# Performance work log

Hardware: AMD Instinct MI355X
Metric: run time of the kernel (lower is better)

## Reference

```python
import jax, jax.numpy as jnp
import numpy as np

N_Q, N_T, D, C = 4096, 8192, 512, 16
SIGMA = 2.0


def setup_inputs() -> dict:
    key = jax.random.key(0)
    k1, k2, k3 = jax.random.split(key, 3)
    X = jax.random.normal(k1, (N_Q, D), dtype=jnp.float32)
    X_train = jax.random.normal(k2, (N_T, D), dtype=jnp.float32)
    y = jax.random.randint(k3, (N_T,), 0, C, dtype=jnp.int32)
    sigma = jnp.float32(SIGMA)
    return {"X": X, "X_train": X_train, "y": y, "sigma": sigma}


def reference(X, X_train, y, sigma):
    xx = jnp.sum(X * X, axis=1, keepdims=True)              # [N_q, 1]
    tt = jnp.sum(X_train * X_train, axis=1)                 # [N_t]
    cross = jnp.einsum('qd,td->qt', X, X_train)             # [N_q, N_t]
    dist2 = jnp.maximum(xx + tt[None, :] - 2.0 * cross, 0.0)
    pattern = jnp.exp(-dist2 / (2.0 * sigma ** 2))          # Gaussian RBF kernel [N_q, N_t]
    # per-class segment sum over training patterns (replaces per-class Python loop)
    summation = jax.ops.segment_sum(pattern.T, y, num_segments=C).T  # [N_q, C]
    summation = summation / jnp.sum(summation, axis=1, keepdims=True)
    return jnp.argmax(summation, axis=1)
```

## Files before the change

### kernel.cpp

```cpp
#include <hip/hip_runtime.h>


#define NQ 4096
#define NT 8192
#define DD 512
#define NC 16
#define LN_FLT_MIN -87.336544750402f
#define SCREEN_T 750.0f

typedef __attribute__((ext_vector_type(4))) int   v4i;
typedef __attribute__((ext_vector_type(8))) int   v8i;
typedef __attribute__((ext_vector_type(16))) float f32x16;

static __device__ __forceinline__ unsigned f2fp4(float x) {
  const float a = __builtin_fabsf(x);
  unsigned i = (unsigned)(a >= 0.25f) + (a >= 0.75f) + (a >= 1.25f)
             + (a >= 1.75f) + (a >= 2.5f) + (a >= 3.5f) + (a >= 5.0f);
  return i | (x < 0.0f ? 8u : 0u);
}

__global__ __launch_bounds__(256) void prep_k(const float* __restrict__ X,
                                              const float* __restrict__ XT,
                                              unsigned char* __restrict__ fXp,
                                              unsigned char* __restrict__ fTp,
                                              float* __restrict__ xx,
                                              float* __restrict__ tt,
                                              float* __restrict__ classacc) {
  const int lane = threadIdx.x & 63;
  const int row  = blockIdx.x * 4 + (threadIdx.x >> 6);
  const float* src; unsigned char* dst; float* nrm; int r;
  if (row < NT) { r = row; src = XT + (size_t)r * DD; dst = fTp; nrm = tt + r; }
  else { r = row - NT; src = X + (size_t)r * DD; dst = fXp; nrm = xx + r; }
  const float4* s4 = (const float4*)src;
  const float4 a = s4[lane * 2], b = s4[lane * 2 + 1];
  const unsigned word =  f2fp4(a.x)        | (f2fp4(a.y) << 4)
                      | (f2fp4(a.z) << 8)  | (f2fp4(a.w) << 12)
                      | (f2fp4(b.x) << 16) | (f2fp4(b.y) << 20)
                      | (f2fp4(b.z) << 24) | (f2fp4(b.w) << 28);
  const int l = (r & 31) + 32 * ((lane >> 2) & 1);
  const size_t dest = ((size_t)(r >> 5) * 8 + (lane >> 3)) * 1024
                    + l * 16 + (lane & 3) * 4;
  *(unsigned*)(dst + dest) = word;
  float acc = a.x*a.x + a.y*a.y + a.z*a.z + a.w*a.w
            + b.x*b.x + b.y*b.y + b.z*b.z + b.w*b.w;
  #pragma unroll
  for (int off = 32; off; off >>= 1) acc += __shfl_down(acc, off, 64);
  if (lane == 0) *nrm = acc;
  if (blockIdx.x < 64) {
    float4 z = {0.f, 0.f, 0.f, 0.f};
    ((float4*)classacc)[blockIdx.x * 256 + threadIdx.x] = z;
  }
}

#define MFMA4(A, B, C) __builtin_amdgcn_mfma_scale_f32_32x32x64_f8f6f4( \
    (A), (B), (C), 4, 4, 0, 127, 0, 127)
#define BAR() __builtin_amdgcn_s_barrier()
#define WAITV(N) asm volatile("s_waitcnt vmcnt(" #N ")" ::: "memory")

static __device__ __forceinline__ void gll(const unsigned char* src, char* dst) {
  __builtin_amdgcn_global_load_lds(
      (const __attribute__((address_space(1))) unsigned int*)src,
      (__attribute__((address_space(3))) unsigned int*)dst, 16, 0, 0);
}

static __device__ __forceinline__ v8i ld16(const char* p) {
  const v4i lo = *(const v4i*)p;
  return __builtin_shufflevector(lo, lo, 0, 1, 2, 3, -1, -1, -1, -1);
}

__global__ __launch_bounds__(512) void pnn_mfma(const unsigned char* __restrict__ fXp,
                                                const unsigned char* __restrict__ fTp,
                                                const float* __restrict__ Xf,
                                                const float* __restrict__ Tf,
                                                const int* __restrict__ y,
                                                const float* __restrict__ sigp,
                                                const float* __restrict__ xx,
                                                const float* __restrict__ tt,
                                                float* __restrict__ classacc) {
  extern __shared__ char lds[];
  const int tid  = threadIdx.x;
  const int w    = tid >> 6, lane = tid & 63;
  const int la   = lane & 31, lb = lane >> 5;
  const int wr   = w >> 2, wc = w & 3;

  const int bid = blockIdx.x;
  const int xcd = bid & 7, cc = bid >> 3;
  const int qt  = (xcd & 3) * 8 + (cc >> 4);
  const int tn  = (xcd >> 2) * 16 + (cc & 15);
  const int qbase = qt * 128, tbase = tn * 256;
  const int qrt0 = qbase >> 5, trt0 = tbase >> 5;

  const unsigned char* sb0 = fXp + ((size_t)(qrt0 + (w >> 1)) * 8 + (w & 1)) * 1024 + lane * 16;
  const unsigned char* sb1 = fTp + ((size_t)(trt0 + (w >> 1)) * 8 + (w & 1)) * 1024 + lane * 16;
  const unsigned char* sb2 = fTp + ((size_t)(trt0 + 4 + (w >> 1)) * 8 + (w & 1)) * 1024 + lane * 16;
  const int d0 = w * 1024 + lane * 16;
  const int d1 = (w + 8) * 1024 + lane * 16;
  const int d2 = (w + 16) * 1024 + lane * 16;

#define STAGE(s, bofs) { \
    gll(sb0 + (size_t)(s) * 2048, lds + (bofs) + d0); \
    gll(sb1 + (size_t)(s) * 2048, lds + (bofs) + d1); \
    gll(sb2 + (size_t)(s) * 2048, lds + (bofs) + d2); }

  f32x16 acc00 = (f32x16)(0.f), acc01 = (f32x16)(0.f);
  f32x16 acc10 = (f32x16)(0.f), acc11 = (f32x16)(0.f);

  STAGE(0, 0)

  #pragma unroll
  for (int s = 0; s < 4; ++s) {
    const int cur = (s % 3) * 24576;
    const int nxt = ((s + 1) % 3) * 24576;
    if (s < 3) { STAGE(s + 1, nxt) }
    if (s < 3) { WAITV(3); } else { WAITV(0); }
    BAR();
    const char* Bp = lds + cur;
    const v8i a00 = ld16(Bp + ((wr * 2 + 0) * 2 + 0) * 1024 + lane * 16);
    const v8i a10 = ld16(Bp + ((wr * 2 + 1) * 2 + 0) * 1024 + lane * 16);
    const v8i b00 = ld16(Bp + (8 + (wc * 2 + 0) * 2 + 0) * 1024 + lane * 16);
    const v8i b10 = ld16(Bp + (8 + (wc * 2 + 1) * 2 + 0) * 1024 + lane * 16);
    const v8i a01 = ld16(Bp + ((wr * 2 + 0) * 2 + 1) * 1024 + lane * 16);
    const v8i a11 = ld16(Bp + ((wr * 2 + 1) * 2 + 1) * 1024 + lane * 16);
    const v8i b01 = ld16(Bp + (8 + (wc * 2 + 0) * 2 + 1) * 1024 + lane * 16);
    const v8i b11 = ld16(Bp + (8 + (wc * 2 + 1) * 2 + 1) * 1024 + lane * 16);
    __builtin_amdgcn_s_setprio(1);
    acc00 = MFMA4(a00, b00, acc00);
    acc01 = MFMA4(a00, b10, acc01);
    acc10 = MFMA4(a10, b00, acc10);
    acc11 = MFMA4(a10, b10, acc11);
    acc00 = MFMA4(a01, b01, acc00);
    acc01 = MFMA4(a01, b11, acc01);
    acc10 = MFMA4(a11, b01, acc10);
    acc11 = MFMA4(a11, b11, acc11);
    __builtin_amdgcn_s_setprio(0);
  }
#undef STAGE

  const int wq = qbase + wr * 64;
  const int wt = tbase + wc * 64;
  const float sg = sigp[0];
  const float inv2s2 = 1.0f / (2.0f * sg * sg);
  float tnorm[2]; int tcls[2];
  #pragma unroll
  for (int nt = 0; nt < 2; ++nt) {
    const int t = wt + nt * 32 + la;
    tnorm[nt] = tt[t]; tcls[nt] = y[t];
  }

#define EPIL(ACC, mt, nt) { \
    _Pragma("unroll") \
    for (int reg = 0; reg < 16; ++reg) { \
      const int q = wq + (mt) * 32 + (reg & 3) + 8 * (reg >> 2) + 4 * lb; \
      const float xq = xx[q]; \
      const float d2 = xq + tnorm[(nt)] - 2.0f * (ACC)[reg]; \
      if (__builtin_expect(d2 < SCREEN_T, 0)) { \
        const int t = wt + (nt) * 32 + la; \
        const float4* xp = (const float4*)(Xf + (size_t)q * DD); \
        const float4* tp = (const float4*)(Tf + (size_t)t * DD); \
        float s0 = 0.f, s1 = 0.f, s2 = 0.f, s3 = 0.f; \
        for (int d = 0; d < DD / 4; ++d) { \
          const float4 xv = xp[d], tv = tp[d]; \
          s0 = fmaf(xv.x, tv.x, s0); s1 = fmaf(xv.y, tv.y, s1); \
          s2 = fmaf(xv.z, tv.z, s2); s3 = fmaf(xv.w, tv.w, s3); \
        } \
        const float dot = (s0 + s1) + (s2 + s3); \
        const float dd2 = fmaxf(xq + tnorm[(nt)] - 2.0f * dot, 0.f); \
        const float arg = -dd2 * inv2s2; \
        if (arg >= LN_FLT_MIN)             \
          atomicAdd(&classacc[q * NC + tcls[(nt)]], expf(arg)); \
      } \
    } }

  EPIL(acc00, 0, 0)
  EPIL(acc01, 0, 1)
  EPIL(acc10, 1, 0)
  EPIL(acc11, 1, 1)
#undef EPIL
}

__global__ __launch_bounds__(256) void argmax_k(const float* __restrict__ classacc,
                                                float* __restrict__ out) {
  const int q = blockIdx.x * 256 + threadIdx.x;
  float sc[NC];
  #pragma unroll
  for (int c4 = 0; c4 < 4; ++c4) {
    const float4 v = ((const float4*)(classacc + (size_t)q * NC))[c4];
    sc[c4*4+0] = v.x; sc[c4*4+1] = v.y; sc[c4*4+2] = v.z; sc[c4*4+3] = v.w;
  }
  float rowsum = 0.f;
  #pragma unroll
  for (int c = 0; c < NC; ++c) rowsum += sc[c];
  int best = 0; float bv = sc[0];
  #pragma unroll
  for (int c = 1; c < NC; ++c)
    if (sc[c] > bv) { bv = sc[c]; best = c; }
  out[q] = (rowsum > 0.f) ? (float)best : 0.0f;
}

extern "C" void kernel_launch(void* const* d_in, const int* in_sizes, int n_in,
                              void* d_out, int out_size, void* d_ws, size_t ws_size,
                              hipStream_t stream) {
  const float* X  = (const float*)d_in[0];
  const float* XT = (const float*)d_in[1];
  const int*   y  = (const int*)d_in[2];
  const float* sg = (const float*)d_in[3];
  float* out = (float*)d_out;

  char* wsp = (char*)d_ws;
  unsigned char* fXp = (unsigned char*)wsp;
  unsigned char* fTp = fXp + (size_t)NQ * DD / 2;
  float* tt       = (float*)(wsp + 4u * 1024u * 1024u);
  float* xx       = tt + NT;
  float* classacc = xx + NQ;

  (void)hipFuncSetAttribute((const void*)pnn_mfma,
                            hipFuncAttributeMaxDynamicSharedMemorySize, 73728);

  prep_k<<<(NQ + NT) / 4, 256, 0, stream>>>(X, XT, fXp, fTp, xx, tt, classacc);
  pnn_mfma<<<1024, 512, 73728, stream>>>(fXp, fTp, X, XT, y, sg, xx, tt, classacc);
  argmax_k<<<NQ / 256, 256, 0, stream>>>(classacc, out);
}
```

Before: 50.98 us.

## Keep query FP4 tile in registers and loop over training strips per block

Each block now holds its 128-query FP4 A tile in registers for the whole K=512 and iterates over four 256-wide training tiles of a 1024-wide strip. Those B tiles are double-buffered in 128KB of LDS, cutting the grid from 1024 to 256 blocks. The aim is to reuse A across training tiles and overlap the next B load with MFMA and epilogue work, avoiding the per-block restaging of A. The cost is one block per CU, so 256 blocks only partly fill the GPU. It also adds more register pressure and serialises the epilogue with compute inside each block.

```diff
diff --git a/kernel.cpp b/kernel.cpp
--- a/kernel.cpp
+++ b/kernel.cpp
@@ -55,7 +55,7 @@
 #define MFMA4(A, B, C) __builtin_amdgcn_mfma_scale_f32_32x32x64_f8f6f4( \
     (A), (B), (C), 4, 4, 0, 127, 0, 127)
 #define BAR() __builtin_amdgcn_s_barrier()
-#define WAITV(N) asm volatile("s_waitcnt vmcnt(" #N ")" ::: "memory")
+#define WAITV0() asm volatile("s_waitcnt vmcnt(0)" ::: "memory")
 
 static __device__ __forceinline__ void gll(const unsigned char* src, char* dst) {
   __builtin_amdgcn_global_load_lds(
@@ -63,89 +63,82 @@
       (__attribute__((address_space(3))) unsigned int*)dst, 16, 0, 0);
 }
 
-static __device__ __forceinline__ v8i ld16(const char* p) {
-  const v4i lo = *(const v4i*)p;
+static __device__ __forceinline__ v8i pk8(v4i lo) {
   return __builtin_shufflevector(lo, lo, 0, 1, 2, 3, -1, -1, -1, -1);
 }
 
-__global__ __launch_bounds__(512) void pnn_mfma(const unsigned char* __restrict__ fXp,
-                                                const unsigned char* __restrict__ fTp,
-                                                const float* __restrict__ Xf,
-                                                const float* __restrict__ Tf,
-                                                const int* __restrict__ y,
-                                                const float* __restrict__ sigp,
-                                                const float* __restrict__ xx,
-                                                const float* __restrict__ tt,
-                                                float* __restrict__ classacc) {
+__global__ __launch_bounds__(512, 1) void pnn_mfma(const unsigned char* __restrict__ fXp,
+                                                   const unsigned char* __restrict__ fTp,
+                                                   const float* __restrict__ Xf,
+                                                   const float* __restrict__ Tf,
+                                                   const int* __restrict__ y,
+                                                   const float* __restrict__ sigp,
+                                                   const float* __restrict__ xx,
+                                                   const float* __restrict__ tt,
+                                                   float* __restrict__ classacc) {
   extern __shared__ char lds[];
   const int tid  = threadIdx.x;
   const int w    = tid >> 6, lane = tid & 63;
   const int la   = lane & 31, lb = lane >> 5;
   const int wr   = w >> 2, wc = w & 3;
 
-  const int bid = blockIdx.x;
-  const int xcd = bid & 7, cc = bid >> 3;
-  const int qt  = (xcd & 3) * 8 + (cc >> 4);
-  const int tn  = (xcd >> 2) * 16 + (cc & 15);
-  const int qbase = qt * 128, tbase = tn * 256;
-  const int qrt0 = qbase >> 5, trt0 = tbase >> 5;
-
-  const unsigned char* sb0 = fXp + ((size_t)(qrt0 + (w >> 1)) * 8 + (w & 1)) * 1024 + lane * 16;
-  const unsigned char* sb1 = fTp + ((size_t)(trt0 + (w >> 1)) * 8 + (w & 1)) * 1024 + lane * 16;
-  const unsigned char* sb2 = fTp + ((size_t)(trt0 + 4 + (w >> 1)) * 8 + (w & 1)) * 1024 + lane * 16;
-  const int d0 = w * 1024 + lane * 16;
-  const int d1 = (w + 8) * 1024 + lane * 16;
-  const int d2 = (w + 16) * 1024 + lane * 16;
-
-#define STAGE(s, bofs) { \
-    gll(sb0 + (size_t)(s) * 2048, lds + (bofs) + d0); \
-    gll(sb1 + (size_t)(s) * 2048, lds + (bofs) + d1); \
-    gll(sb2 + (size_t)(s) * 2048, lds + (bofs) + d2); }
-
-  f32x16 acc00 = (f32x16)(0.f), acc01 = (f32x16)(0.f);
-  f32x16 acc10 = (f32x16)(0.f), acc11 = (f32x16)(0.f);
-
-  STAGE(0, 0)
-
-  #pragma unroll
-  for (int s = 0; s < 4; ++s) {
-    const int cur = (s % 3) * 24576;
-    const int nxt = ((s + 1) % 3) * 24576;
-    if (s < 3) { STAGE(s + 1, nxt) }
-    if (s < 3) { WAITV(3); } else { WAITV(0); }
-    BAR();
-    const char* Bp = lds + cur;
-    const v8i a00 = ld16(Bp + ((wr * 2 + 0) * 2 + 0) * 1024 + lane * 16);
-    const v8i a10 = ld16(Bp + ((wr * 2 + 1) * 2 + 0) * 1024 + lane * 16);
-    const v8i b00 = ld16(Bp + (8 + (wc * 2 + 0) * 2 + 0) * 1024 + lane * 16);
-    const v8i b10 = ld16(Bp + (8 + (wc * 2 + 1) * 2 + 0) * 1024 + lane * 16);
-    const v8i a01 = ld16(Bp + ((wr * 2 + 0) * 2 + 1) * 1024 + lane * 16);
-    const v8i a11 = ld16(Bp + ((wr * 2 + 1) * 2 + 1) * 1024 + lane * 16);
-    const v8i b01 = ld16(Bp + (8 + (wc * 2 + 0) * 2 + 1) * 1024 + lane * 16);
-    const v8i b11 = ld16(Bp + (8 + (wc * 2 + 1) * 2 + 1) * 1024 + lane * 16);
-    __builtin_amdgcn_s_setprio(1);
-    acc00 = MFMA4(a00, b00, acc00);
-    acc01 = MFMA4(a00, b10, acc01);
-    acc10 = MFMA4(a10, b00, acc10);
-    acc11 = MFMA4(a10, b10, acc11);
-    acc00 = MFMA4(a01, b01, acc00);
-    acc01 = MFMA4(a01, b11, acc01);
-    acc10 = MFMA4(a11, b01, acc10);
-    acc11 = MFMA4(a11, b11, acc11);
-    __builtin_amdgcn_s_setprio(0);
-  }
-#undef STAGE
-
-  const int wq = qbase + wr * 64;
-  const int wt = tbase + wc * 64;
+  const int bid   = blockIdx.x;
+  const int strip = bid & 7;
+  const int qt    = bid >> 3;
+  const int qbase = qt * 128;
+  const int rt0   = (qbase >> 5) + wr * 2;
+
   const float sg = sigp[0];
   const float inv2s2 = 1.0f / (2.0f * sg * sg);
-  float tnorm[2]; int tcls[2];
-  #pragma unroll
-  for (int nt = 0; nt < 2; ++nt) {
-    const int t = wt + nt * 32 + la;
-    tnorm[nt] = tt[t]; tcls[nt] = y[t];
-  }
+  const int wq = qbase + wr * 64;
+
+  v4i av[2][8];
+  #pragma unroll
+  for (int mt = 0; mt < 2; ++mt)
+    #pragma unroll
+    for (int kt = 0; kt < 8; ++kt)
+      av[mt][kt] = *(const v4i*)(fXp + ((size_t)(rt0 + mt) * 8 + kt) * 1024 + lane * 16);
+
+#define STAGEB(buf, trt0) { \
+    _Pragma("unroll") \
+    for (int j = 0; j < 8; ++j) \
+      gll(fTp + ((size_t)((trt0) + j) * 8 + w) * 1024 + lane * 16, \
+          (buf) + (j * 8 + w) * 1024 + lane * 16); }
+
+  char* cur = lds;
+  char* nxt = lds + 65536;
+
+  STAGEB(cur, strip * 32)
+  WAITV0();
+  BAR();
+
+  #pragma clang loop unroll(disable)
+  for (int t = 0; t < 4; ++t) {
+    if (t < 3) STAGEB(nxt, strip * 32 + (t + 1) * 8)
+
+    f32x16 acc00 = (f32x16)(0.f), acc01 = (f32x16)(0.f);
+    f32x16 acc10 = (f32x16)(0.f), acc11 = (f32x16)(0.f);
+
+    #pragma unroll
+    for (int kt = 0; kt < 8; ++kt) {
+      const v4i b0 = *(const v4i*)(cur + ((wc * 2 + 0) * 8 + kt) * 1024 + lane * 16);
+      const v4i b1 = *(const v4i*)(cur + ((wc * 2 + 1) * 8 + kt) * 1024 + lane * 16);
+      const v8i a0 = pk8(av[0][kt]), a1 = pk8(av[1][kt]);
+      const v8i bb0 = pk8(b0), bb1 = pk8(b1);
+      acc00 = MFMA4(a0, bb0, acc00);
+      acc01 = MFMA4(a0, bb1, acc01);
+      acc10 = MFMA4(a1, bb0, acc10);
+      acc11 = MFMA4(a1, bb1, acc11);
+    }
+
+    const int tbase = strip * 1024 + t * 256;
+    const int wt = tbase + wc * 64;
+    float tnorm[2]; int tcls[2];
+    #pragma unroll
+    for (int nt = 0; nt < 2; ++nt) {
+      const int tg = wt + nt * 32 + la;
+      tnorm[nt] = tt[tg]; tcls[nt] = y[tg];
+    }
 
 #define EPIL(ACC, mt, nt) { \
     _Pragma("unroll") \
@@ -154,9 +147,9 @@
       const float xq = xx[q]; \
       const float d2 = xq + tnorm[(nt)] - 2.0f * (ACC)[reg]; \
       if (__builtin_expect(d2 < SCREEN_T, 0)) { \
-        const int t = wt + (nt) * 32 + la; \
+        const int tg = wt + (nt) * 32 + la; \
         const float4* xp = (const float4*)(Xf + (size_t)q * DD); \
-        const float4* tp = (const float4*)(Tf + (size_t)t * DD); \
+        const float4* tp = (const float4*)(Tf + (size_t)tg * DD); \
         float s0 = 0.f, s1 = 0.f, s2 = 0.f, s3 = 0.f; \
         for (int d = 0; d < DD / 4; ++d) { \
           const float4 xv = xp[d], tv = tp[d]; \
@@ -171,11 +164,17 @@
       } \
     } }
 
-  EPIL(acc00, 0, 0)
-  EPIL(acc01, 0, 1)
-  EPIL(acc10, 1, 0)
-  EPIL(acc11, 1, 1)
+    EPIL(acc00, 0, 0)
+    EPIL(acc01, 0, 1)
+    EPIL(acc10, 1, 0)
+    EPIL(acc11, 1, 1)
 #undef EPIL
+
+    WAITV0();
+    BAR();
+    char* tmp = cur; cur = nxt; nxt = tmp;
+  }
+#undef STAGEB
 }
 
 __global__ __launch_bounds__(256) void argmax_k(const float* __restrict__ classacc,
@@ -214,9 +213,9 @@
   float* classacc = xx + NQ;
 
   (void)hipFuncSetAttribute((const void*)pnn_mfma,
-                            hipFuncAttributeMaxDynamicSharedMemorySize, 73728);
+                            hipFuncAttributeMaxDynamicSharedMemorySize, 131072);
 
   prep_k<<<(NQ + NT) / 4, 256, 0, stream>>>(X, XT, fXp, fTp, xx, tt, classacc);
-  pnn_mfma<<<1024, 512, 73728, stream>>>(fXp, fTp, X, XT, y, sg, xx, tt, classacc);
+  pnn_mfma<<<256, 512, 131072, stream>>>(fXp, fTp, X, XT, y, sg, xx, tt, classacc);
   argmax_k<<<NQ / 256, 256, 0, stream>>>(classacc, out);
 }
```

Result: faster. 45.35 us, median of 2 (-11.0%).
